# Performance work log

Measured on AMD Instinct MI355X. Metric: run time of the kernel, lower is better.

The kernel has to match this reference:

```python
import jax, jax.numpy as jnp
import numpy as np
import math

NODE_DIM = 256
HIDDEN = 128
HEADS = 8
HEAD_DIM = HIDDEN // HEADS
SCALE = math.sqrt(HEAD_DIM)
EPS_DIST = 1e-6
EPS_NORM = 1e-6
LN_EPS = 1e-5


def setup_inputs() -> dict:
    key = jax.random.key(0)
    ks = jax.random.split(key, 16)
    B, N = 2, 768
    node_feats = jax.random.normal(ks[0], (B, N, NODE_DIM), dtype=jnp.float32)
    positions = jax.random.normal(ks[1], (B, N, 2), dtype=jnp.float32)
    mask = jax.random.randint(ks[2], (B, N), 0, 2).astype(bool)
    s = 0.05
    return {
        "node_feats": node_feats,
        "positions": positions,
        "mask": mask,
        "Wq": jax.random.normal(ks[3], (NODE_DIM, HIDDEN), dtype=jnp.float32) * s,
        "Wk": jax.random.normal(ks[4], (NODE_DIM, HIDDEN), dtype=jnp.float32) * s,
        "Wv": jax.random.normal(ks[5], (NODE_DIM, HIDDEN), dtype=jnp.float32) * s,
        "W1": jax.random.normal(ks[6], (3, HIDDEN), dtype=jnp.float32) * s,
        "b1": jnp.zeros((HIDDEN,), dtype=jnp.float32),
        "W2": jax.random.normal(ks[7], (HIDDEN, HIDDEN), dtype=jnp.float32) * s,
        "b2": jnp.zeros((HIDDEN,), dtype=jnp.float32),
        "Wo": jax.random.normal(ks[8], (HIDDEN, NODE_DIM), dtype=jnp.float32) * s,
        "bo": jnp.zeros((NODE_DIM,), dtype=jnp.float32),
        "gamma": jnp.ones((NODE_DIM,), dtype=jnp.float32),
        "beta": jnp.zeros((NODE_DIM,), dtype=jnp.float32),
    }


def reference(node_feats, positions, mask, Wq, Wk, Wv, W1, b1, W2, b2, Wo, bo, gamma, beta):
    B, N, _ = node_feats.shape
    # projections -> [B, H, N, hd]
    q = (node_feats @ Wq).reshape(B, N, HEADS, HEAD_DIM).transpose(0, 2, 1, 3)
    k = (node_feats @ Wk).reshape(B, N, HEADS, HEAD_DIM).transpose(0, 2, 1, 3)
    v = (node_feats @ Wv).reshape(B, N, HEADS, HEAD_DIM).transpose(0, 2, 1, 3)

    # pairwise geometry: deltas [B, N, N, 2]
    deltas = positions[:, :, None, :] - positions[:, None, :, :]
    sq = (deltas ** 2).sum(-1)
    distances = jnp.sqrt(sq + EPS_DIST)  # [B, N, N]
    # F.normalize: divide by norm clamped to eps
    norm = jnp.sqrt(sq)[..., None]
    direction = deltas / jnp.maximum(norm, EPS_NORM)
    edge_geom = jnp.concatenate([direction, distances[..., None]], axis=-1)  # [B,N,N,3]

    # edge MLP -> [B, N, N, HIDDEN] (exact GELU as torch default)
    h = jax.nn.gelu(edge_geom @ W1 + b1, approximate=False)
    edge_bias = (h @ W2 + b2).reshape(B, N, N, HEADS, HEAD_DIM)
    # mean over head_dim, permute to [B, H, N, N]
    bias = edge_bias.mean(-1).transpose(0, 3, 1, 2)

    scores = jnp.einsum('bhid,bhjd->bhij', q, k) / SCALE + bias

    key_mask = mask[:, None, None, :]  # [B,1,1,N]
    neg = jnp.finfo(scores.dtype).min
    scores = jnp.where(key_mask, scores, neg)
    valid_key_rows = jnp.any(key_mask, axis=-1, keepdims=True)  # [B,1,1,1]

    mx = scores.max(axis=-1, keepdims=True)
    mx = jnp.where(valid_key_rows, mx, 0.0)
    scores = jnp.where(valid_key_rows, scores - mx, 0.0)
    w = jax.nn.softmax(scores, axis=-1)
    w = jnp.where(valid_key_rows, w, 0.0)
    w = jnp.nan_to_num(w, nan=0.0, posinf=0.0, neginf=0.0)
    # query mask
    w = w * mask[:, None, :, None].astype(w.dtype)
    # dropout is identity at eval time

    agg = jnp.einsum('bhij,bhjd->bhid', w, v)  # [B,H,N,hd]
    agg = agg.transpose(0, 2, 1, 3).reshape(B, N, HIDDEN)
    agg = agg @ Wo + bo

    mf = mask[..., None].astype(node_feats.dtype)
    agg = agg * mf
    nf = node_feats * mf

    x = nf + agg
    mu = x.mean(-1, keepdims=True)
    var = ((x - mu) ** 2).mean(-1, keepdims=True)
    return (x - mu) / jnp.sqrt(var + LN_EPS) * gamma + beta
```

## Files before the change

### kernel.cpp

```cpp
#include <hip/hip_runtime.h>
#include <float.h>
#include <math.h>

#define NODE_DIM 256
#define HIDDEN   128
#define HEADS    8
#define HEAD_DIM 16
#define NB       768
#define BATCH    2
#define NNODES   (BATCH * NB)
#define SEP      776

typedef _Float16 f16;

__device__ __forceinline__ float gelu_f(float u) {
  float u2 = u * u;
  float m  = u * fmaf(u2, -0.0713548162f, -1.5957691216f);
  float e  = __expf(m);
  return u * __builtin_amdgcn_rcpf(1.0f + e);
}

__global__ __launch_bounds__(256) void setup_kernel(
    const int* __restrict__ mask, const float* __restrict__ pos,
    const float* __restrict__ W1, const float* __restrict__ b1,
    const float* __restrict__ W2, const float* __restrict__ b2,
    int* __restrict__ cnt, int* __restrict__ cidx, int* __restrict__ vlist,
    int* __restrict__ mlist, float* __restrict__ pcx, float* __restrict__ pcy,
    float* __restrict__ kTc, float* __restrict__ P, float* __restrict__ b2m) {
  int blk = blockIdx.x, t = threadIdx.x;
  if (blk < 2) {
    int b = blk;
    __shared__ int cs, ms;
    __shared__ int lst[NB], mlst[NB];
    if (t == 0) { cs = 0; ms = 0; }
    __syncthreads();
    for (int j = t; j < NB; j += 256) {
      if (mask[b * NB + j] != 0) { int p = atomicAdd(&cs, 1); lst[p] = j; }
      else                       { int p = atomicAdd(&ms, 1); mlst[p] = j; }
    }
    __syncthreads();
    int nv = cs;
    if (t == 0) cnt[b] = nv;
    for (int i = t; i < nv; i += 256) {
      int j = lst[i];
      cidx[b * NB + j] = i;
      vlist[b * NB + i] = j;
      pcx[b * NB + i] = pos[(b * NB + j) * 2];
      pcy[b * NB + i] = pos[(b * NB + j) * 2 + 1];
    }
    for (int i = t; i < NB - nv; i += 256) mlist[b * NB + i] = mlst[i];
    int nvp = (nv + 3) & ~3;
    if (nvp > nv && t < HIDDEN) {
      for (int col = nv; col < nvp; ++col)
        kTc[((size_t)b * HIDDEN + t) * NB + col] = 0.0f;
    }
  } else {
    __shared__ float w2s[HIDDEN * HEADS];
    for (int idx = t; idx < HIDDEN * HEADS; idx += 256) {
      int c = idx >> 3, h = idx & 7;
      float s = 0.0f;
      for (int d = 0; d < HEAD_DIM; ++d) s += W2[c * HIDDEN + h * HEAD_DIM + d];
      w2s[idx] = s * (1.0f / 16.0f);
    }
    if (t < HEADS) {
      float s = 0.0f;
      for (int d = 0; d < HEAD_DIM; ++d) s += b2[t * HEAD_DIM + d];
      b2m[t] = s * (1.0f / 16.0f);
    }
    __syncthreads();
    if (t < HIDDEN) {
      float* Pr = P + t * 12;
      Pr[0] = W1[t];
      Pr[1] = W1[HIDDEN + t];
      Pr[2] = W1[2 * HIDDEN + t];
      Pr[3] = b1[t];
#pragma unroll
      for (int h = 0; h < HEADS; ++h) Pr[4 + h] = w2s[t * 8 + h];
    }
  }
}

__global__ __launch_bounds__(256) void qkv_kernel(
    const float* __restrict__ nf, const float* __restrict__ Wq,
    const float* __restrict__ Wk, const float* __restrict__ Wv,
    const int* __restrict__ mask, const int* __restrict__ cidx,
    float* __restrict__ qc, float* __restrict__ kTc, float* __restrict__ vc) {
  int n0 = blockIdx.x * 2;
  int t = threadIdx.x;
  const float* x0 = nf + (size_t)(n0 + 0) * NODE_DIM;
  const float* x1 = nf + (size_t)(n0 + 1) * NODE_DIM;
  for (int id = t; id < 3 * HIDDEN; id += 256) {
    int m = id >> 7, c = id & 127;
    const float* W = (m == 0) ? Wq : (m == 1) ? Wk : Wv;
    float a0 = 0.f, b0 = 0.f, a1 = 0.f, b1_ = 0.f;
#pragma unroll 8
    for (int kk = 0; kk < NODE_DIM; kk += 2) {
      float w0 = W[kk * HIDDEN + c];
      float w1 = W[(kk + 1) * HIDDEN + c];
      a0 = fmaf(x0[kk], w0, a0);  b0 = fmaf(x0[kk + 1], w1, b0);
      a1 = fmaf(x1[kk], w0, a1);  b1_ = fmaf(x1[kk + 1], w1, b1_);
    }
    float acc[2] = {a0 + b0, a1 + b1_};
#pragma unroll
    for (int n = 0; n < 2; ++n) {
      int node = n0 + n;
      if (mask[node] != 0) {
        int b = node / NB;
        int ci = cidx[node];
        int slot = b * NB + ci;
        if (m == 0)      qc[(size_t)slot * HIDDEN + c] = acc[n];
        else if (m == 1) kTc[((size_t)b * HIDDEN + c) * NB + ci] = acc[n];
        else             vc[(size_t)slot * HIDDEN + c] = acc[n];
      }
    }
  }
}

__global__ __launch_bounds__(256) void attn_kernel(
    const float* __restrict__ pcx, const float* __restrict__ pcy,
    const int* __restrict__ cnt, const int* __restrict__ vlist,
    const int* __restrict__ mlist, const float* __restrict__ P,
    const float* __restrict__ b2m, const float* __restrict__ qc,
    const float* __restrict__ kTc, const float* __restrict__ vc,
    const float* __restrict__ nf, const float* __restrict__ Wo,
    const float* __restrict__ bo, const float* __restrict__ gamma,
    const float* __restrict__ beta, float* __restrict__ out) {
  int x = blockIdx.x;
  int b = x & 1, ci = x >> 1;
  int nv = cnt[b];
  int t = threadIdx.x;

  if (ci >= nv) {
    int node = b * NB + mlist[b * NB + (ci - nv)];
    out[(size_t)node * NODE_DIM + t] = beta[t];
    return;
  }
  int node = b * NB + vlist[b * NB + ci];
  int slot = b * NB + ci;

  __shared__ f16  sE0[HEADS][SEP];
  __shared__ f16  sE1[HEADS][SEP];
  __shared__ __align__(16) float qs[HIDDEN];
  __shared__ float invs[HEADS];
  __shared__ float partD[8][HIDDEN];
  __shared__ __align__(16) float aggL[HIDDEN];
  __shared__ float red[2][4];

  if (t < HIDDEN) qs[t] = qc[(size_t)slot * HIDDEN + t];
  float pix = pcx[slot], piy = pcy[slot];
  __syncthreads();

  {
    int h = t >> 5, l = t & 31;
    const float* kb = kTc + ((size_t)b * HIDDEN + h * 16) * NB;
    float qv[16];
#pragma unroll
    for (int r = 0; r < 16; ++r) qv[r] = qs[h * 16 + r];
    float bh = b2m[h];
    int nvp4 = (nv + 3) >> 2;
    for (int j4 = l; j4 < nvp4; j4 += 32) {
      float4 acc = {0.f, 0.f, 0.f, 0.f};
#pragma unroll
      for (int r = 0; r < 16; ++r) {
        float4 kv = ((const float4*)(kb + (size_t)r * NB))[j4];
        acc.x = fmaf(qv[r], kv.x, acc.x);
        acc.y = fmaf(qv[r], kv.y, acc.y);
        acc.z = fmaf(qv[r], kv.z, acc.z);
        acc.w = fmaf(qv[r], kv.w, acc.w);
      }
      sE0[h][4 * j4 + 0] = (f16)fmaf(acc.x, 0.25f, bh);
      sE0[h][4 * j4 + 1] = (f16)fmaf(acc.y, 0.25f, bh);
      sE0[h][4 * j4 + 2] = (f16)fmaf(acc.z, 0.25f, bh);
      sE0[h][4 * j4 + 3] = (f16)fmaf(acc.w, 0.25f, bh);
    }
  }
  __syncthreads();

  {
    int kk = t & 127, ch = t >> 7;
    int cb = ch * 64;
    for (int base = 0; base < nv; base += 384) {
      int k0 = base + kk;
      if (k0 >= nv) continue;
      int k1 = k0 + 128, k2 = k0 + 256;
      bool v1 = k1 < nv, v2 = k2 < nv;
      int s0 = b * NB + k0;
      int s1 = b * NB + (v1 ? k1 : k0);
      int s2 = b * NB + (v2 ? k2 : k0);
      float ux0, uy0, dd0, ux1, uy1, dd1, ux2, uy2, dd2;
      {
        float dx = pix - pcx[s0], dy = piy - pcy[s0];
        float sq = dx * dx + dy * dy;
        dd0 = sqrtf(sq + 1e-6f);
        float dn = fmaxf(sqrtf(sq), 1e-6f);
        ux0 = dx / dn; uy0 = dy / dn;
      }
      {
        float dx = pix - pcx[s1], dy = piy - pcy[s1];
        float sq = dx * dx + dy * dy;
        dd1 = sqrtf(sq + 1e-6f);
        float dn = fmaxf(sqrtf(sq), 1e-6f);
        ux1 = dx / dn; uy1 = dy / dn;
      }
      {
        float dx = pix - pcx[s2], dy = piy - pcy[s2];
        float sq = dx * dx + dy * dy;
        dd2 = sqrtf(sq + 1e-6f);
        float dn = fmaxf(sqrtf(sq), 1e-6f);
        ux2 = dx / dn; uy2 = dy / dn;
      }
      float bias0[8] = {}, bias1[8] = {}, bias2[8] = {};
#pragma unroll 4
      for (int c = cb; c < cb + 64; ++c) {
        const float4* Pc = (const float4*)(P + c * 12);
        float4 p0 = Pc[0], p1 = Pc[1], p2 = Pc[2];
        float g0 = gelu_f(fmaf(ux0, p0.x, fmaf(uy0, p0.y, fmaf(dd0, p0.z, p0.w))));
        float g1 = gelu_f(fmaf(ux1, p0.x, fmaf(uy1, p0.y, fmaf(dd1, p0.z, p0.w))));
        float g2 = gelu_f(fmaf(ux2, p0.x, fmaf(uy2, p0.y, fmaf(dd2, p0.z, p0.w))));
        bias0[0]=fmaf(g0,p1.x,bias0[0]); bias1[0]=fmaf(g1,p1.x,bias1[0]); bias2[0]=fmaf(g2,p1.x,bias2[0]);
        bias0[1]=fmaf(g0,p1.y,bias0[1]); bias1[1]=fmaf(g1,p1.y,bias1[1]); bias2[1]=fmaf(g2,p1.y,bias2[1]);
        bias0[2]=fmaf(g0,p1.z,bias0[2]); bias1[2]=fmaf(g1,p1.z,bias1[2]); bias2[2]=fmaf(g2,p1.z,bias2[2]);
        bias0[3]=fmaf(g0,p1.w,bias0[3]); bias1[3]=fmaf(g1,p1.w,bias1[3]); bias2[3]=fmaf(g2,p1.w,bias2[3]);
        bias0[4]=fmaf(g0,p2.x,bias0[4]); bias1[4]=fmaf(g1,p2.x,bias1[4]); bias2[4]=fmaf(g2,p2.x,bias2[4]);
        bias0[5]=fmaf(g0,p2.y,bias0[5]); bias1[5]=fmaf(g1,p2.y,bias1[5]); bias2[5]=fmaf(g2,p2.y,bias2[5]);
        bias0[6]=fmaf(g0,p2.z,bias0[6]); bias1[6]=fmaf(g1,p2.z,bias1[6]); bias2[6]=fmaf(g2,p2.z,bias2[6]);
        bias0[7]=fmaf(g0,p2.w,bias0[7]); bias1[7]=fmaf(g1,p2.w,bias1[7]); bias2[7]=fmaf(g2,p2.w,bias2[7]);
      }
      if (ch == 0) {
#pragma unroll
        for (int h = 0; h < 8; ++h) sE0[h][k0] = (f16)((float)sE0[h][k0] + bias0[h]);
        if (v1) {
#pragma unroll
          for (int h = 0; h < 8; ++h) sE0[h][k1] = (f16)((float)sE0[h][k1] + bias1[h]);
        }
        if (v2) {
#pragma unroll
          for (int h = 0; h < 8; ++h) sE0[h][k2] = (f16)((float)sE0[h][k2] + bias2[h]);
        }
      } else {
#pragma unroll
        for (int h = 0; h < 8; ++h) sE1[h][k0] = (f16)bias0[h];
        if (v1) {
#pragma unroll
          for (int h = 0; h < 8; ++h) sE1[h][k1] = (f16)bias1[h];
        }
        if (v2) {
#pragma unroll
          for (int h = 0; h < 8; ++h) sE1[h][k2] = (f16)bias2[h];
        }
      }
    }
  }
  __syncthreads();

  {
    int h = t >> 5, l = t & 31;
    float m = -FLT_MAX;
    for (int jj = l; jj < nv; jj += 32)
      m = fmaxf(m, (float)sE0[h][jj] + (float)sE1[h][jj]);
    for (int off = 16; off; off >>= 1) m = fmaxf(m, __shfl_down(m, off, 32));
    m = __shfl(m, 0, 32);
    float s = 0.0f;
    for (int jj = l; jj < nv; jj += 32) {
      float e = __expf((float)sE0[h][jj] + (float)sE1[h][jj] - m);
      sE0[h][jj] = (f16)e;
      s += e;
    }
    for (int off = 16; off; off >>= 1) s += __shfl_down(s, off, 32);
    if (l == 0) invs[h] = 1.0f / s;
  }
  __syncthreads();

  {
    int o4 = t & 31, g = t >> 3 >> 2;
    g = t >> 5;
    int h = o4 >> 2;
    float4 acc = {0.f, 0.f, 0.f, 0.f};
    for (int jj = g; jj < nv; jj += 8) {
      float w = (float)sE0[h][jj];
      float4 vv = ((const float4*)(vc + ((size_t)(b * NB + jj)) * HIDDEN))[o4];
      acc.x = fmaf(w, vv.x, acc.x);
      acc.y = fmaf(w, vv.y, acc.y);
      acc.z = fmaf(w, vv.z, acc.z);
      acc.w = fmaf(w, vv.w, acc.w);
    }
    ((float4*)&partD[g][o4 * 4])[0] = acc;
  }
  __syncthreads();
  if (t < HIDDEN) {
    float s = 0.0f;
#pragma unroll
    for (int g = 0; g < 8; ++g) s += partD[g][t];
    aggL[t] = s * invs[t >> 4];
  }
  __syncthreads();

  {
    float y0 = bo[t], y1 = 0.f, y2 = 0.f, y3 = 0.f;
    const float4* a4 = (const float4*)aggL;
#pragma unroll 4
    for (int kg = 0; kg < 32; ++kg) {
      float4 a = a4[kg];
      y0 = fmaf(a.x, Wo[(4 * kg + 0) * NODE_DIM + t], y0);
      y1 = fmaf(a.y, Wo[(4 * kg + 1) * NODE_DIM + t], y1);
      y2 = fmaf(a.z, Wo[(4 * kg + 2) * NODE_DIM + t], y2);
      y3 = fmaf(a.w, Wo[(4 * kg + 3) * NODE_DIM + t], y3);
    }
    float y = (y0 + y1) + (y2 + y3);
    float xv = nf[(size_t)node * NODE_DIM + t] + y;
    float s = xv, s2 = xv * xv;
    for (int off = 32; off; off >>= 1) {
      s += __shfl_down(s, off, 64);
      s2 += __shfl_down(s2, off, 64);
    }
    if ((t & 63) == 0) { red[0][t >> 6] = s; red[1][t >> 6] = s2; }
    __syncthreads();
    s  = red[0][0] + red[0][1] + red[0][2] + red[0][3];
    s2 = red[1][0] + red[1][1] + red[1][2] + red[1][3];
    float mu = s * (1.0f / NODE_DIM);
    float var = fmaxf(s2 * (1.0f / NODE_DIM) - mu * mu, 0.0f);
    out[(size_t)node * NODE_DIM + t] =
        (xv - mu) * rsqrtf(var + 1e-5f) * gamma[t] + beta[t];
  }
}

extern "C" void kernel_launch(void* const* d_in, const int* in_sizes, int n_in,
                              void* d_out, int out_size, void* d_ws, size_t ws_size,
                              hipStream_t stream) {
  const float* nf    = (const float*)d_in[0];
  const float* pos   = (const float*)d_in[1];
  const int*   mask  = (const int*)  d_in[2];
  const float* Wq    = (const float*)d_in[3];
  const float* Wk    = (const float*)d_in[4];
  const float* Wv    = (const float*)d_in[5];
  const float* W1    = (const float*)d_in[6];
  const float* b1    = (const float*)d_in[7];
  const float* W2    = (const float*)d_in[8];
  const float* b2    = (const float*)d_in[9];
  const float* Wo    = (const float*)d_in[10];
  const float* bo    = (const float*)d_in[11];
  const float* gamma = (const float*)d_in[12];
  const float* beta  = (const float*)d_in[13];

  const int QKV = NNODES * HIDDEN;

  float* ws   = (float*)d_ws;
  float* qc   = ws;
  float* kTc  = qc + QKV;
  float* vc   = kTc + QKV;
  float* P    = vc + QKV;
  float* b2m  = P + HIDDEN * 12;
  float* pcx  = b2m + 8;
  float* pcy  = pcx + NNODES;
  int*   cidx = (int*)(pcy + NNODES);
  int*   vlist= cidx + NNODES;
  int*   mlist= vlist + NNODES;
  int*   cnt  = mlist + NNODES;

  setup_kernel<<<3,          256, 0, stream>>>(mask, pos, W1, b1, W2, b2,
                                               cnt, cidx, vlist, mlist,
                                               pcx, pcy, kTc, P, b2m);
  qkv_kernel  <<<NNODES / 2, 256, 0, stream>>>(nf, Wq, Wk, Wv, mask, cidx,
                                               qc, kTc, vc);
  attn_kernel <<<2 * NB,     256, 0, stream>>>(pcx, pcy, cnt, vlist, mlist,
                                               P, b2m, qc, kTc, vc,
                                               nf, Wo, bo, gamma, beta,
                                               (float*)d_out);
}
```

Baseline: 140.8 us.

## Merge setup and QKV kernels, use packed fp16 edge-MLP bias accumulation

Merges the setup and QKV projection kernels into one prep kernel. Each QKV block now computes its compacted index itself with a ballot prefix count instead of reading cidx, which removes a launch and the dependency between the two. The edge-MLP bias loop changes from splitting 128 channels over two thread halves with a second fp16 buffer to one thread per key. That thread accumulates the 8 head biases with packed half2 FMAs, using exp2 and rsq intrinsics. Shared memory shrinks, which may help occupancy, but fp16 accumulation over 128 channels costs precision.

```diff
diff --git a/kernel.cpp b/kernel.cpp
--- a/kernel.cpp
+++ b/kernel.cpp
@@ -12,48 +12,116 @@
 #define SEP      776
 
 typedef _Float16 f16;
+typedef _Float16 h2 __attribute__((ext_vector_type(2)));
+union F2H { float f; h2 h; };
 
 __device__ __forceinline__ float gelu_f(float u) {
   float u2 = u * u;
-  float m  = u * fmaf(u2, -0.0713548162f, -1.5957691216f);
-  float e  = __expf(m);
+  float e  = __builtin_amdgcn_exp2f(u * fmaf(u2, -0.10294357f, -2.3022090f));
   return u * __builtin_amdgcn_rcpf(1.0f + e);
 }
 
-__global__ __launch_bounds__(256) void setup_kernel(
-    const int* __restrict__ mask, const float* __restrict__ pos,
-    const float* __restrict__ W1, const float* __restrict__ b1,
-    const float* __restrict__ W2, const float* __restrict__ b2,
-    int* __restrict__ cnt, int* __restrict__ cidx, int* __restrict__ vlist,
-    int* __restrict__ mlist, float* __restrict__ pcx, float* __restrict__ pcy,
-    float* __restrict__ kTc, float* __restrict__ P, float* __restrict__ b2m) {
+__global__ __launch_bounds__(256) void prep_kernel(
+    const float* __restrict__ nf, const float* __restrict__ pos,
+    const int* __restrict__ mask,
+    const float* __restrict__ Wq, const float* __restrict__ Wk,
+    const float* __restrict__ Wv, const float* __restrict__ W1,
+    const float* __restrict__ b1, const float* __restrict__ W2,
+    const float* __restrict__ b2,
+    float* __restrict__ qc, float* __restrict__ kTc, float* __restrict__ vc,
+    float* __restrict__ P, float* __restrict__ b2m,
+    float* __restrict__ pcx, float* __restrict__ pcy,
+    int* __restrict__ vlist, int* __restrict__ mlist, int* __restrict__ cnt) {
   int blk = blockIdx.x, t = threadIdx.x;
-  if (blk < 2) {
-    int b = blk;
-    __shared__ int cs, ms;
-    __shared__ int lst[NB], mlst[NB];
-    if (t == 0) { cs = 0; ms = 0; }
-    __syncthreads();
-    for (int j = t; j < NB; j += 256) {
-      if (mask[b * NB + j] != 0) { int p = atomicAdd(&cs, 1); lst[p] = j; }
-      else                       { int p = atomicAdd(&ms, 1); mlst[p] = j; }
-    }
-    __syncthreads();
-    int nv = cs;
+
+  if (blk < NNODES / 4) {
+    int n0 = blk * 4;
+    int b = n0 / NB;
+    int lo = n0 - b * NB;
+    __shared__ int accv;
+    if (t == 0) accv = 0;
+    __syncthreads();
+    for (int jb = 0; jb < lo; jb += 256) {
+      int j = jb + t;
+      int mv = (j < lo) && (mask[b * NB + j] != 0);
+      unsigned long long ball = __ballot(mv);
+      if ((t & 63) == 0) atomicAdd(&accv, __popcll(ball));
+    }
+    __syncthreads();
+    int cb = accv;
+    int m0 = mask[n0] != 0, m1 = mask[n0 + 1] != 0, m2 = mask[n0 + 2] != 0,
+        m3 = mask[n0 + 3] != 0;
+    int civ[4] = {cb, cb + m0, cb + m0 + m1, cb + m0 + m1 + m2};
+    int mv4[4] = {m0, m1, m2, m3};
+
+    const float* x0 = nf + (size_t)(n0 + 0) * NODE_DIM;
+    const float* x1 = nf + (size_t)(n0 + 1) * NODE_DIM;
+    const float* x2 = nf + (size_t)(n0 + 2) * NODE_DIM;
+    const float* x3 = nf + (size_t)(n0 + 3) * NODE_DIM;
+    for (int id = t; id < 3 * HIDDEN; id += 256) {
+      int m = id >> 7, c = id & 127;
+      const float* W = (m == 0) ? Wq : (m == 1) ? Wk : Wv;
+      float a0 = 0.f, a1 = 0.f, a2 = 0.f, a3 = 0.f;
+      float e0 = 0.f, e1 = 0.f, e2 = 0.f, e3 = 0.f;
+#pragma unroll 8
+      for (int kk = 0; kk < NODE_DIM; kk += 2) {
+        float w0 = W[kk * HIDDEN + c];
+        float w1 = W[(kk + 1) * HIDDEN + c];
+        a0 = fmaf(x0[kk], w0, a0);  e0 = fmaf(x0[kk + 1], w1, e0);
+        a1 = fmaf(x1[kk], w0, a1);  e1 = fmaf(x1[kk + 1], w1, e1);
+        a2 = fmaf(x2[kk], w0, a2);  e2 = fmaf(x2[kk + 1], w1, e2);
+        a3 = fmaf(x3[kk], w0, a3);  e3 = fmaf(x3[kk + 1], w1, e3);
+      }
+      float acc[4] = {a0 + e0, a1 + e1, a2 + e2, a3 + e3};
+#pragma unroll
+      for (int n = 0; n < 4; ++n) {
+        if (mv4[n]) {
+          int slot = b * NB + civ[n];
+          if (m == 0)      qc[(size_t)slot * HIDDEN + c] = acc[n];
+          else if (m == 1) kTc[((size_t)b * HIDDEN + c) * NB + civ[n]] = acc[n];
+          else             vc[(size_t)slot * HIDDEN + c] = acc[n];
+        }
+      }
+    }
+  } else if (blk < NNODES / 4 + 2) {
+    int b = blk - NNODES / 4;
+    __shared__ int wcnt[4];
+    __shared__ int base2[2];
+    if (t < 2) base2[t] = 0;
+    __syncthreads();
+    int lane = t & 63, w = t >> 6;
+    for (int iter = 0; iter < NB / 256; ++iter) {
+      int j = iter * 256 + t;
+      int mv = mask[b * NB + j] != 0;
+      unsigned long long ball = __ballot(mv);
+      if (lane == 0) wcnt[w] = __popcll(ball);
+      __syncthreads();
+      int pv = 0;
+      for (int i = 0; i < w; ++i) pv += wcnt[i];
+      int pin = (lane == 0) ? 0 : __popcll(ball & (~0ull >> (64 - lane)));
+      if (mv) {
+        int p = base2[0] + pv + pin;
+        vlist[b * NB + p] = j;
+        pcx[b * NB + p] = pos[(b * NB + j) * 2];
+        pcy[b * NB + p] = pos[(b * NB + j) * 2 + 1];
+      } else {
+        int pm = base2[1] + (w * 64 - pv) + (lane - pin);
+        mlist[b * NB + pm] = j;
+      }
+      __syncthreads();
+      if (t == 0) {
+        int tot = wcnt[0] + wcnt[1] + wcnt[2] + wcnt[3];
+        base2[0] += tot;
+        base2[1] += 256 - tot;
+      }
+      __syncthreads();
+    }
+    int nv = base2[0];
     if (t == 0) cnt[b] = nv;
-    for (int i = t; i < nv; i += 256) {
-      int j = lst[i];
-      cidx[b * NB + j] = i;
-      vlist[b * NB + i] = j;
-      pcx[b * NB + i] = pos[(b * NB + j) * 2];
-      pcy[b * NB + i] = pos[(b * NB + j) * 2 + 1];
-    }
-    for (int i = t; i < NB - nv; i += 256) mlist[b * NB + i] = mlst[i];
     int nvp = (nv + 3) & ~3;
-    if (nvp > nv && t < HIDDEN) {
+    if (t < HIDDEN)
       for (int col = nv; col < nvp; ++col)
         kTc[((size_t)b * HIDDEN + t) * NB + col] = 0.0f;
-    }
   } else {
     __shared__ float w2s[HIDDEN * HEADS];
     for (int idx = t; idx < HIDDEN * HEADS; idx += 256) {
@@ -69,49 +137,14 @@
     }
     __syncthreads();
     if (t < HIDDEN) {
-      float* Pr = P + t * 12;
+      float* Pr = P + t * 8;
       Pr[0] = W1[t];
       Pr[1] = W1[HIDDEN + t];
       Pr[2] = W1[2 * HIDDEN + t];
       Pr[3] = b1[t];
-#pragma unroll
-      for (int h = 0; h < HEADS; ++h) Pr[4 + h] = w2s[t * 8 + h];
-    }
-  }
-}
-
-__global__ __launch_bounds__(256) void qkv_kernel(
-    const float* __restrict__ nf, const float* __restrict__ Wq,
-    const float* __restrict__ Wk, const float* __restrict__ Wv,
-    const int* __restrict__ mask, const int* __restrict__ cidx,
-    float* __restrict__ qc, float* __restrict__ kTc, float* __restrict__ vc) {
-  int n0 = blockIdx.x * 2;
-  int t = threadIdx.x;
-  const float* x0 = nf + (size_t)(n0 + 0) * NODE_DIM;
-  const float* x1 = nf + (size_t)(n0 + 1) * NODE_DIM;
-  for (int id = t; id < 3 * HIDDEN; id += 256) {
-    int m = id >> 7, c = id & 127;
-    const float* W = (m == 0) ? Wq : (m == 1) ? Wk : Wv;
-    float a0 = 0.f, b0 = 0.f, a1 = 0.f, b1_ = 0.f;
-#pragma unroll 8
-    for (int kk = 0; kk < NODE_DIM; kk += 2) {
-      float w0 = W[kk * HIDDEN + c];
-      float w1 = W[(kk + 1) * HIDDEN + c];
-      a0 = fmaf(x0[kk], w0, a0);  b0 = fmaf(x0[kk + 1], w1, b0);
-      a1 = fmaf(x1[kk], w0, a1);  b1_ = fmaf(x1[kk + 1], w1, b1_);
-    }
-    float acc[2] = {a0 + b0, a1 + b1_};
-#pragma unroll
-    for (int n = 0; n < 2; ++n) {
-      int node = n0 + n;
-      if (mask[node] != 0) {
-        int b = node / NB;
-        int ci = cidx[node];
-        int slot = b * NB + ci;
-        if (m == 0)      qc[(size_t)slot * HIDDEN + c] = acc[n];
-        else if (m == 1) kTc[((size_t)b * HIDDEN + c) * NB + ci] = acc[n];
-        else             vc[(size_t)slot * HIDDEN + c] = acc[n];
-      }
+      f16* ph = (f16*)(Pr + 4);
+#pragma unroll
+      for (int h = 0; h < HEADS; ++h) ph[h] = (f16)w2s[t * 8 + h];
     }
   }
 }
@@ -125,11 +158,9 @@
     const float* __restrict__ nf, const float* __restrict__ Wo,
     const float* __restrict__ bo, const float* __restrict__ gamma,
     const float* __restrict__ beta, float* __restrict__ out) {
-  int x = blockIdx.x;
-  int b = x & 1, ci = x >> 1;
+  int b = blockIdx.x & 1, ci = blockIdx.x >> 1;
+  int t = threadIdx.x;
   int nv = cnt[b];
-  int t = threadIdx.x;
-
   if (ci >= nv) {
     int node = b * NB + mlist[b * NB + (ci - nv)];
     out[(size_t)node * NODE_DIM + t] = beta[t];
@@ -138,13 +169,13 @@
   int node = b * NB + vlist[b * NB + ci];
   int slot = b * NB + ci;
 
-  __shared__ f16  sE0[HEADS][SEP];
-  __shared__ f16  sE1[HEADS][SEP];
-  __shared__ __align__(16) float qs[HIDDEN];
-  __shared__ float invs[HEADS];
-  __shared__ float partD[8][HIDDEN];
-  __shared__ __align__(16) float aggL[HIDDEN];
-  __shared__ float red[2][4];
+  __shared__ __align__(16) unsigned char smem[17600];
+  f16*   sE    = (f16*)smem;
+  float* qs    = (float*)(smem + 12416);
+  float* partD = (float*)(smem + 12928);
+  float* aggL  = (float*)(smem + 17024);
+  float* red   = (float*)(smem + 17536);
+  float* invs  = (float*)(smem + 17568);
 
   if (t < HIDDEN) qs[t] = qc[(size_t)slot * HIDDEN + t];
   float pix = pcx[slot], piy = pcy[slot];
@@ -168,102 +199,63 @@
         acc.z = fmaf(qv[r], kv.z, acc.z);
         acc.w = fmaf(qv[r], kv.w, acc.w);
       }
-      sE0[h][4 * j4 + 0] = (f16)fmaf(acc.x, 0.25f, bh);
-      sE0[h][4 * j4 + 1] = (f16)fmaf(acc.y, 0.25f, bh);
-      sE0[h][4 * j4 + 2] = (f16)fmaf(acc.z, 0.25f, bh);
-      sE0[h][4 * j4 + 3] = (f16)fmaf(acc.w, 0.25f, bh);
-    }
-  }
-  __syncthreads();
-
-  {
-    int kk = t & 127, ch = t >> 7;
-    int cb = ch * 64;
-    for (int base = 0; base < nv; base += 384) {
-      int k0 = base + kk;
-      if (k0 >= nv) continue;
-      int k1 = k0 + 128, k2 = k0 + 256;
-      bool v1 = k1 < nv, v2 = k2 < nv;
+      sE[h * SEP + 4 * j4 + 0] = (f16)fmaf(acc.x, 0.25f, bh);
+      sE[h * SEP + 4 * j4 + 1] = (f16)fmaf(acc.y, 0.25f, bh);
+      sE[h * SEP + 4 * j4 + 2] = (f16)fmaf(acc.z, 0.25f, bh);
+      sE[h * SEP + 4 * j4 + 3] = (f16)fmaf(acc.w, 0.25f, bh);
+    }
+  }
+  __syncthreads();
+
+#pragma unroll
+  for (int sl = 0; sl < 3; ++sl) {
+    int k0 = t + sl * 256;
+    if (k0 < nv) {
       int s0 = b * NB + k0;
-      int s1 = b * NB + (v1 ? k1 : k0);
-      int s2 = b * NB + (v2 ? k2 : k0);
-      float ux0, uy0, dd0, ux1, uy1, dd1, ux2, uy2, dd2;
-      {
-        float dx = pix - pcx[s0], dy = piy - pcy[s0];
-        float sq = dx * dx + dy * dy;
-        dd0 = sqrtf(sq + 1e-6f);
-        float dn = fmaxf(sqrtf(sq), 1e-6f);
-        ux0 = dx / dn; uy0 = dy / dn;
-      }
-      {
-        float dx = pix - pcx[s1], dy = piy - pcy[s1];
-        float sq = dx * dx + dy * dy;
-        dd1 = sqrtf(sq + 1e-6f);
-        float dn = fmaxf(sqrtf(sq), 1e-6f);
-        ux1 = dx / dn; uy1 = dy / dn;
-      }
-      {
-        float dx = pix - pcx[s2], dy = piy - pcy[s2];
-        float sq = dx * dx + dy * dy;
-        dd2 = sqrtf(sq + 1e-6f);
-        float dn = fmaxf(sqrtf(sq), 1e-6f);
-        ux2 = dx / dn; uy2 = dy / dn;
-      }
-      float bias0[8] = {}, bias1[8] = {}, bias2[8] = {};
+      float dx = pix - pcx[s0], dy = piy - pcy[s0];
+      float sq = fmaf(dx, dx, dy * dy);
+      float dist = __builtin_amdgcn_sqrtf(sq + 1e-6f);
+      float inv  = fminf(__builtin_amdgcn_rsqf(sq), 1e6f);
+      float ux = dx * inv, uy = dy * inv;
+      h2 b01 = {0, 0}, b23 = {0, 0}, b45 = {0, 0}, b67 = {0, 0};
 #pragma unroll 4
-      for (int c = cb; c < cb + 64; ++c) {
-        const float4* Pc = (const float4*)(P + c * 12);
-        float4 p0 = Pc[0], p1 = Pc[1], p2 = Pc[2];
-        float g0 = gelu_f(fmaf(ux0, p0.x, fmaf(uy0, p0.y, fmaf(dd0, p0.z, p0.w))));
-        float g1 = gelu_f(fmaf(ux1, p0.x, fmaf(uy1, p0.y, fmaf(dd1, p0.z, p0.w))));
-        float g2 = gelu_f(fmaf(ux2, p0.x, fmaf(uy2, p0.y, fmaf(dd2, p0.z, p0.w))));
-        bias0[0]=fmaf(g0,p1.x,bias0[0]); bias1[0]=fmaf(g1,p1.x,bias1[0]); bias2[0]=fmaf(g2,p1.x,bias2[0]);
-        bias0[1]=fmaf(g0,p1.y,bias0[1]); bias1[1]=fmaf(g1,p1.y,bias1[1]); bias2[1]=fmaf(g2,p1.y,bias2[1]);
-        bias0[2]=fmaf(g0,p1.z,bias0[2]); bias1[2]=fmaf(g1,p1.z,bias1[2]); bias2[2]=fmaf(g2,p1.z,bias2[2]);
-        bias0[3]=fmaf(g0,p1.w,bias0[3]); bias1[3]=fmaf(g1,p1.w,bias1[3]); bias2[3]=fmaf(g2,p1.w,bias2[3]);
-        bias0[4]=fmaf(g0,p2.x,bias0[4]); bias1[4]=fmaf(g1,p2.x,bias1[4]); bias2[4]=fmaf(g2,p2.x,bias2[4]);
-        bias0[5]=fmaf(g0,p2.y,bias0[5]); bias1[5]=fmaf(g1,p2.y,bias1[5]); bias2[5]=fmaf(g2,p2.y,bias2[5]);
-        bias0[6]=fmaf(g0,p2.z,bias0[6]); bias1[6]=fmaf(g1,p2.z,bias1[6]); bias2[6]=fmaf(g2,p2.z,bias2[6]);
-        bias0[7]=fmaf(g0,p2.w,bias0[7]); bias1[7]=fmaf(g1,p2.w,bias1[7]); bias2[7]=fmaf(g2,p2.w,bias2[7]);
-      }
-      if (ch == 0) {
-#pragma unroll
-        for (int h = 0; h < 8; ++h) sE0[h][k0] = (f16)((float)sE0[h][k0] + bias0[h]);
-        if (v1) {
-#pragma unroll
-          for (int h = 0; h < 8; ++h) sE0[h][k1] = (f16)((float)sE0[h][k1] + bias1[h]);
-        }
-        if (v2) {
-#pragma unroll
-          for (int h = 0; h < 8; ++h) sE0[h][k2] = (f16)((float)sE0[h][k2] + bias2[h]);
-        }
-      } else {
-#pragma unroll
-        for (int h = 0; h < 8; ++h) sE1[h][k0] = (f16)bias0[h];
-        if (v1) {
-#pragma unroll
-          for (int h = 0; h < 8; ++h) sE1[h][k1] = (f16)bias1[h];
-        }
-        if (v2) {
-#pragma unroll
-          for (int h = 0; h < 8; ++h) sE1[h][k2] = (f16)bias2[h];
-        }
-      }
+      for (int c = 0; c < HIDDEN; ++c) {
+        const float4* Pc = (const float4*)(P + c * 8);
+        float4 p0 = Pc[0], pw = Pc[1];
+        float g = gelu_f(fmaf(ux, p0.x, fmaf(uy, p0.y, fmaf(dist, p0.z, p0.w))));
+        f16 gh = (f16)g;
+        h2 gg = {gh, gh};
+        F2H w0, w1, w2, w3;
+        w0.f = pw.x; w1.f = pw.y; w2.f = pw.z; w3.f = pw.w;
+        b01 += gg * w0.h;
+        b23 += gg * w1.h;
+        b45 += gg * w2.h;
+        b67 += gg * w3.h;
+      }
+      f16* row = sE + k0;
+      row[0 * SEP] = (f16)(row[0 * SEP] + b01.x);
+      row[1 * SEP] = (f16)(row[1 * SEP] + b01.y);
+      row[2 * SEP] = (f16)(row[2 * SEP] + b23.x);
+      row[3 * SEP] = (f16)(row[3 * SEP] + b23.y);
+      row[4 * SEP] = (f16)(row[4 * SEP] + b45.x);
+      row[5 * SEP] = (f16)(row[5 * SEP] + b45.y);
+      row[6 * SEP] = (f16)(row[6 * SEP] + b67.x);
+      row[7 * SEP] = (f16)(row[7 * SEP] + b67.y);
     }
   }
   __syncthreads();
 
   {
     int h = t >> 5, l = t & 31;
+    f16* row = sE + h * SEP;
     float m = -FLT_MAX;
-    for (int jj = l; jj < nv; jj += 32)
-      m = fmaxf(m, (float)sE0[h][jj] + (float)sE1[h][jj]);
+    for (int jj = l; jj < nv; jj += 32) m = fmaxf(m, (float)row[jj]);
     for (int off = 16; off; off >>= 1) m = fmaxf(m, __shfl_down(m, off, 32));
     m = __shfl(m, 0, 32);
     float s = 0.0f;
     for (int jj = l; jj < nv; jj += 32) {
-      float e = __expf((float)sE0[h][jj] + (float)sE1[h][jj] - m);
-      sE0[h][jj] = (f16)e;
+      float e = __expf((float)row[jj] - m);
+      row[jj] = (f16)e;
       s += e;
     }
     for (int off = 16; off; off >>= 1) s += __shfl_down(s, off, 32);
@@ -272,25 +264,24 @@
   __syncthreads();
 
   {
-    int o4 = t & 31, g = t >> 3 >> 2;
-    g = t >> 5;
+    int o4 = t & 31, g = t >> 5;
     int h = o4 >> 2;
     float4 acc = {0.f, 0.f, 0.f, 0.f};
     for (int jj = g; jj < nv; jj += 8) {
-      float w = (float)sE0[h][jj];
+      float w = (float)sE[h * SEP + jj];
       float4 vv = ((const float4*)(vc + ((size_t)(b * NB + jj)) * HIDDEN))[o4];
       acc.x = fmaf(w, vv.x, acc.x);
       acc.y = fmaf(w, vv.y, acc.y);
       acc.z = fmaf(w, vv.z, acc.z);
       acc.w = fmaf(w, vv.w, acc.w);
     }
-    ((float4*)&partD[g][o4 * 4])[0] = acc;
+    ((float4*)(partD + g * HIDDEN + o4 * 4))[0] = acc;
   }
   __syncthreads();
   if (t < HIDDEN) {
     float s = 0.0f;
 #pragma unroll
-    for (int g = 0; g < 8; ++g) s += partD[g][t];
+    for (int g = 0; g < 8; ++g) s += partD[g * HIDDEN + t];
     aggL[t] = s * invs[t >> 4];
   }
   __syncthreads();
@@ -313,10 +304,10 @@
       s += __shfl_down(s, off, 64);
       s2 += __shfl_down(s2, off, 64);
     }
-    if ((t & 63) == 0) { red[0][t >> 6] = s; red[1][t >> 6] = s2; }
-    __syncthreads();
-    s  = red[0][0] + red[0][1] + red[0][2] + red[0][3];
-    s2 = red[1][0] + red[1][1] + red[1][2] + red[1][3];
+    if ((t & 63) == 0) { red[t >> 6] = s; red[4 + (t >> 6)] = s2; }
+    __syncthreads();
+    s  = red[0] + red[1] + red[2] + red[3];
+    s2 = red[4] + red[5] + red[6] + red[7];
     float mu = s * (1.0f / NODE_DIM);
     float var = fmaxf(s2 * (1.0f / NODE_DIM) - mu * mu, 0.0f);
     out[(size_t)node * NODE_DIM + t] =
@@ -349,21 +340,17 @@
   float* kTc  = qc + QKV;
   float* vc   = kTc + QKV;
   float* P    = vc + QKV;
-  float* b2m  = P + HIDDEN * 12;
+  float* b2m  = P + HIDDEN * 8;
   float* pcx  = b2m + 8;
   float* pcy  = pcx + NNODES;
-  int*   cidx = (int*)(pcy + NNODES);
-  int*   vlist= cidx + NNODES;
+  int*   vlist= (int*)(pcy + NNODES);
   int*   mlist= vlist + NNODES;
   int*   cnt  = mlist + NNODES;
 
-  setup_kernel<<<3,          256, 0, stream>>>(mask, pos, W1, b1, W2, b2,
-                                               cnt, cidx, vlist, mlist,
-                                               pcx, pcy, kTc, P, b2m);
-  qkv_kernel  <<<NNODES / 2, 256, 0, stream>>>(nf, Wq, Wk, Wv, mask, cidx,
-                                               qc, kTc, vc);
-  attn_kernel <<<2 * NB,     256, 0, stream>>>(pcx, pcy, cnt, vlist, mlist,
-                                               P, b2m, qc, kTc, vc,
-                                               nf, Wo, bo, gamma, beta,
-                                               (float*)d_out);
+  prep_kernel<<<NNODES / 4 + 3, 256, 0, stream>>>(
+      nf, pos, mask, Wq, Wk, Wv, W1, b1, W2, b2,
+      qc, kTc, vc, P, b2m, pcx, pcy, vlist, mlist, cnt);
+  attn_kernel<<<NNODES, 256, 0, stream>>>(
+      pcx, pcy, cnt, vlist, mlist, P, b2m, qc, kTc, vc,
+      nf, Wo, bo, gamma, beta, (float*)d_out);
 }
```

Result: slower. 148.9 us (+5.8%).
